# Performance work log

Hardware: AMD Instinct MI355X
Metric: run time of the kernel (lower is better)

The kernel has to match this reference:

```python
import jax, jax.numpy as jnp
import numpy as np

EPS = 1e-5

def _layer_norm(x, w, b):
    mu = jnp.mean(x, axis=-1, keepdims=True)
    var = jnp.mean((x - mu) ** 2, axis=-1, keepdims=True)
    return (x - mu) * jax.lax.rsqrt(var + EPS) * w + b

B, N, C, D = 8, 16384, 256, 2
K = 4096  # ceil(N / 4)

def setup_inputs() -> dict:
    key = jax.random.key(0)
    k0, k1, k2, k3 = jax.random.split(key, 4)
    pos = jax.random.uniform(k0, (B, N, D), dtype=jnp.float32)
    feat = jax.random.normal(k1, (B, N, C), dtype=jnp.float32)
    assignment = jax.random.randint(k2, (B, N), 0, K)
    norm_w = jnp.ones((C + D,), jnp.float32)
    norm_b = jnp.zeros((C + D,), jnp.float32)
    lin_w = jax.random.normal(k3, (2 * C, C + D), jnp.float32) * 0.02
    return {"pos": pos, "feat": feat, "assignment": assignment,
            "norm_w": norm_w, "norm_b": norm_b, "lin_w": lin_w}

def reference(pos, feat, assignment, norm_w, norm_b, lin_w):
    b, n, c = feat.shape
    d = pos.shape[2]
    k = K
    # normalize coordinates by per-dim global max
    pos = pos / jnp.max(pos.reshape(-1, d), axis=0)
    # flatten (batch, cluster) into segments for one big segment_sum
    seg = (assignment + jnp.arange(b, dtype=assignment.dtype)[:, None] * k).reshape(-1)  # [b*n]
    count = jax.ops.segment_sum(jnp.ones((b * n,), pos.dtype), seg,
                                num_segments=b * k).reshape(b, k)
    safe = jnp.maximum(count, 1.0)
    # cluster mean position (scatter_add + divide)
    mean_pos = jax.ops.segment_sum(pos.reshape(-1, d), seg,
                                   num_segments=b * k).reshape(b, k, d) / safe[..., None]
    # relative position via gather
    idx = jnp.broadcast_to(assignment[:, :, None], (b, n, d))
    rel_pos = pos - jnp.take_along_axis(mean_pos, idx, axis=1)
    # norm + linear (dim+pos_dim -> 2*dim, no bias)
    h = _layer_norm(jnp.concatenate([feat, rel_pos], axis=-1), norm_w, norm_b)
    h = jnp.einsum('bnf,of->bno', h, lin_w)  # [b, n, 2c]
    # cluster mean pooling of features (segment sum / count)
    merged = jax.ops.segment_sum(h.reshape(b * n, 2 * c), seg,
                                 num_segments=b * k).reshape(b, k, 2 * c) / safe[..., None]
    # zero out empty clusters and emit validity mask (valid_row_idx path)
    valid = (count > 0).astype(merged.dtype)  # [b, k]
    new_feat = merged * valid[..., None]
    new_pos = mean_pos * valid[..., None]
    new_mask = valid[..., None]  # [b, k, 1]
    return (new_pos, new_feat, new_mask)
```

## Files before the change

kernel.cpp:

```cpp
#include <hip/hip_runtime.h>

#define BB 8
#define NN 16384
#define CC 256
#define KK 4096
#define FDIM 258
#define FP 320
#define OC 512
#define NPTS (BB * NN)
#define NROWS (BB * KK)
#define CAP 64
#define LNEPS 1e-5f

#define OUT_FEAT_OFF 65536
#define OUT_MASK_OFF (65536 + 16777216)

#define OFF_MAX 0
#define OFF_ICOUNT 16
#define OFF_ACCH 32784
#define ACC_FSLOTS (NROWS * FP / 2)
#define OFF_INV (OFF_ACCH + ACC_FSLOTS)
#define OFF_LIST (OFF_INV + NROWS)
#define OFF_WPH (OFF_LIST + NROWS * CAP)
#define ZERO_FLOATS (OFF_ACCH + ACC_FSLOTS)

typedef _Float16 h8v __attribute__((ext_vector_type(8)));
typedef _Float16 h4v __attribute__((ext_vector_type(4)));
typedef float f4v __attribute__((ext_vector_type(4)));

__global__ void k_maxpos(const float* __restrict__ pos, float* ws) {
    int i = blockIdx.x * blockDim.x + threadIdx.x;
    float mx = 0.f, my = 0.f;
    for (; i < NPTS; i += gridDim.x * blockDim.x) {
        float2 p = ((const float2*)pos)[i];
        mx = fmaxf(mx, p.x);
        my = fmaxf(my, p.y);
    }
    for (int off = 32; off > 0; off >>= 1) {
        mx = fmaxf(mx, __shfl_down(mx, off));
        my = fmaxf(my, __shfl_down(my, off));
    }
    if ((threadIdx.x & 63) == 0) {
        atomicMax((int*)(ws + OFF_MAX + 0), __float_as_int(mx));
        atomicMax((int*)(ws + OFF_MAX + 1), __float_as_int(my));
    }
}

__global__ void k_count(const int* __restrict__ asg, float* ws) {
    int* icount = (int*)(ws + OFF_ICOUNT);
    int* list = (int*)(ws + OFF_LIST);
    int i = blockIdx.x * blockDim.x + threadIdx.x;
    for (; i < NPTS; i += gridDim.x * blockDim.x) {
        int b = i >> 14;
        int row = b * KK + asg[i];
        int slot = atomicAdd(icount + row, 1);
        if (slot < CAP) list[row * CAP + slot] = i;
    }
}

__global__ void k_padw(const float* __restrict__ lw, float* ws) {
    _Float16* Wh = (_Float16*)(ws + OFF_WPH);
    int i = blockIdx.x * blockDim.x + threadIdx.x;
    if (i >= OC * FP) return;
    int o = i / FP, f = i - o * FP;
    Wh[i] = (f < FDIM) ? (_Float16)lw[o * FDIM + f] : (_Float16)0.f;
}

__global__ __launch_bounds__(256) void k_gather(
    const float* __restrict__ feat, const float* __restrict__ pos,
    const float* __restrict__ nw, const float* __restrict__ nb,
    float* ws, float* __restrict__ out) {
    int t = threadIdx.x;
    int lane = t & 63;
    int row = (blockIdx.x << 2) + (t >> 6);
    const int* icount = (const int*)(ws + OFF_ICOUNT);
    const int* list = (const int*)(ws + OFF_LIST);
    _Float16* Ah = (_Float16*)(ws + OFF_ACCH);

    int cnt = icount[row];
    if (cnt > CAP) cnt = CAP;
    float fcnt = (float)cnt;
    float invc = 1.f / fmaxf(fcnt, 1.f);
    float mxx = ws[OFF_MAX + 0], mxy = ws[OFF_MAX + 1];

    int ptl = (lane < cnt) ? list[row * CAP + lane] : 0;
    float px = 0.f, py = 0.f;
    if (lane < cnt) {
        float2 p = ((const float2*)pos)[ptl];
        px = p.x / mxx;
        py = p.y / mxy;
    }
    float sx = px, sy = py;
    for (int m = 32; m; m >>= 1) {
        sx += __shfl_xor(sx, m);
        sy += __shfl_xor(sy, m);
    }
    float meanx = sx * invc, meany = sy * invc;
    float valid = (cnt > 0) ? 1.f : 0.f;
    if (lane == 0) {
        out[2 * row + 0] = meanx * valid;
        out[2 * row + 1] = meany * valid;
        out[OUT_MASK_OFF + row] = valid;
        ws[OFF_INV + row] = invc;
    }

    float a0 = 0.f, a1 = 0.f, a2 = 0.f, a3 = 0.f, arx = 0.f, ary = 0.f;
    for (int s = 0; s < cnt; ++s) {
        int pt = __shfl(ptl, s);
        float rx = __shfl(px, s) - meanx;
        float ry = __shfl(py, s) - meany;
        float4 v = ((const float4*)(feat + (size_t)pt * CC))[lane];
        float S = v.x + v.y + v.z + v.w;
        float Q = v.x * v.x + v.y * v.y + v.z * v.z + v.w * v.w;
        for (int m = 32; m; m >>= 1) {
            S += __shfl_xor(S, m);
            Q += __shfl_xor(Q, m);
        }
        S += rx + ry;
        Q += rx * rx + ry * ry;
        float mu = S * (1.f / FDIM);
        float var = Q * (1.f / FDIM) - mu * mu;
        float rs = rsqrtf(var + LNEPS);
        a0 += (v.x - mu) * rs;
        a1 += (v.y - mu) * rs;
        a2 += (v.z - mu) * rs;
        a3 += (v.w - mu) * rs;
        arx += (rx - mu) * rs;
        ary += (ry - mu) * rs;
    }
    float4 w4 = ((const float4*)nw)[lane];
    float4 b4 = ((const float4*)nb)[lane];
    h4v h;
    h[0] = (_Float16)(a0 * w4.x + fcnt * b4.x);
    h[1] = (_Float16)(a1 * w4.y + fcnt * b4.y);
    h[2] = (_Float16)(a2 * w4.z + fcnt * b4.z);
    h[3] = (_Float16)(a3 * w4.w + fcnt * b4.w);
    *(h4v*)(Ah + (size_t)row * FP + lane * 4) = h;
    if (lane == 0) {
        Ah[(size_t)row * FP + 256] = (_Float16)(arx * nw[256] + fcnt * nb[256]);
        Ah[(size_t)row * FP + 257] = (_Float16)(ary * nw[257] + fcnt * nb[257]);
    }
}

#define GM 128
#define GN 128
#define GK 64
#define LDK 72

__global__ __launch_bounds__(256) void k_gemm(const float* __restrict__ ws,
                                              float* __restrict__ out) {
    __shared__ _Float16 As[GM][LDK];
    __shared__ _Float16 Bs[GN][LDK];
    const _Float16* Ah = (const _Float16*)(ws + OFF_ACCH);
    const _Float16* Wh = (const _Float16*)(ws + OFF_WPH);
    const float* inv = ws + OFF_INV;

    int t = threadIdx.x;
    int lane = t & 63;
    int wv = t >> 6;
    int wr = wv & 1, wc = wv >> 1;
    int row0 = blockIdx.x * GM, col0 = blockIdx.y * GN;
    int l15 = lane & 15, kq = lane >> 4;

    f4v acc[4][4] = {};

    for (int k0 = 0; k0 < FP; k0 += GK) {
#pragma unroll
        for (int l = 0; l < 4; ++l) {
            int c = l * 256 + t;
            int r = c >> 3, kb = (c & 7) * 8;
            *(uint4*)&As[r][kb] = *(const uint4*)(Ah + (size_t)(row0 + r) * FP + k0 + kb);
            *(uint4*)&Bs[r][kb] = *(const uint4*)(Wh + (size_t)(col0 + r) * FP + k0 + kb);
        }
        __syncthreads();
#pragma unroll
        for (int ks = 0; ks < 2; ++ks) {
            h8v af[4], bf[4];
#pragma unroll
            for (int i = 0; i < 4; ++i)
                af[i] = *(const h8v*)&As[wr * 64 + i * 16 + l15][ks * 32 + kq * 8];
#pragma unroll
            for (int j = 0; j < 4; ++j)
                bf[j] = *(const h8v*)&Bs[wc * 64 + j * 16 + l15][ks * 32 + kq * 8];
#pragma unroll
            for (int i = 0; i < 4; ++i)
#pragma unroll
                for (int j = 0; j < 4; ++j)
                    acc[i][j] = __builtin_amdgcn_mfma_f32_16x16x32_f16(
                        af[i], bf[j], acc[i][j], 0, 0, 0);
        }
        __syncthreads();
    }

#pragma unroll
    for (int i = 0; i < 4; ++i) {
#pragma unroll
        for (int r = 0; r < 4; ++r) {
            int row = row0 + wr * 64 + i * 16 + kq * 4 + r;
            float sc = inv[row];
#pragma unroll
            for (int j = 0; j < 4; ++j) {
                int col = col0 + wc * 64 + j * 16 + l15;
                out[OUT_FEAT_OFF + (size_t)row * OC + col] = acc[i][j][r] * sc;
            }
        }
    }
}

extern "C" void kernel_launch(void* const* d_in, const int* in_sizes, int n_in,
                              void* d_out, int out_size, void* d_ws, size_t ws_size,
                              hipStream_t stream) {
    const float* pos = (const float*)d_in[0];
    const float* feat = (const float*)d_in[1];
    const int* asg = (const int*)d_in[2];
    const float* nw = (const float*)d_in[3];
    const float* nb = (const float*)d_in[4];
    const float* lw = (const float*)d_in[5];
    float* out = (float*)d_out;
    float* ws = (float*)d_ws;

    hipMemsetAsync(d_ws, 0, (size_t)ZERO_FLOATS * sizeof(float), stream);
    k_maxpos<<<512, 256, 0, stream>>>(pos, ws);
    k_count<<<1024, 256, 0, stream>>>(asg, ws);
    k_padw<<<(OC * FP + 255) / 256, 256, 0, stream>>>(lw, ws);
    k_gather<<<NROWS / 4, 256, 0, stream>>>(feat, pos, nw, nb, ws, out);
    k_gemm<<<dim3(NROWS / GM, OC / GN), 256, 0, stream>>>(ws, out);
}
```

Measured before the change: 317.0 us.

## Fuse prep kernels, shrink workspace memset, swizzle GEMM LDS tiles

Merges max-position, counting, and weight-padding into one prep kernel, removing two launches. The memset now clears only the max and count region; k_gather writes the zero padding columns of the activation buffer itself instead of relying on the large memset. The GEMM drops the padded LDS stride and uses an XOR swizzle on 16-byte chunks to avoid bank conflicts. The risk is in correctness of the padding writes and the swizzle indexing.

```diff
diff --git a/kernel.cpp b/kernel.cpp
--- a/kernel.cpp
+++ b/kernel.cpp
@@ -17,53 +17,53 @@
 
 #define OFF_MAX 0
 #define OFF_ICOUNT 16
+#define MEMSET_FLOATS (16 + NROWS)
 #define OFF_ACCH 32784
 #define ACC_FSLOTS (NROWS * FP / 2)
 #define OFF_INV (OFF_ACCH + ACC_FSLOTS)
 #define OFF_LIST (OFF_INV + NROWS)
 #define OFF_WPH (OFF_LIST + NROWS * CAP)
-#define ZERO_FLOATS (OFF_ACCH + ACC_FSLOTS)
 
 typedef _Float16 h8v __attribute__((ext_vector_type(8)));
 typedef _Float16 h4v __attribute__((ext_vector_type(4)));
 typedef float f4v __attribute__((ext_vector_type(4)));
 
-__global__ void k_maxpos(const float* __restrict__ pos, float* ws) {
-    int i = blockIdx.x * blockDim.x + threadIdx.x;
-    float mx = 0.f, my = 0.f;
-    for (; i < NPTS; i += gridDim.x * blockDim.x) {
+#define PREP_PB 512
+#define PREP_WB 160
+
+__global__ __launch_bounds__(256) void k_prep(const float* __restrict__ pos,
+                                              const int* __restrict__ asg,
+                                              const float* __restrict__ lw,
+                                              float* ws) {
+    int bid = blockIdx.x;
+    if (bid < PREP_PB) {
+        int i = bid * 256 + threadIdx.x;
+        int* icount = (int*)(ws + OFF_ICOUNT);
+        int* list = (int*)(ws + OFF_LIST);
         float2 p = ((const float2*)pos)[i];
-        mx = fmaxf(mx, p.x);
-        my = fmaxf(my, p.y);
-    }
-    for (int off = 32; off > 0; off >>= 1) {
-        mx = fmaxf(mx, __shfl_down(mx, off));
-        my = fmaxf(my, __shfl_down(my, off));
-    }
-    if ((threadIdx.x & 63) == 0) {
-        atomicMax((int*)(ws + OFF_MAX + 0), __float_as_int(mx));
-        atomicMax((int*)(ws + OFF_MAX + 1), __float_as_int(my));
-    }
-}
-
-__global__ void k_count(const int* __restrict__ asg, float* ws) {
-    int* icount = (int*)(ws + OFF_ICOUNT);
-    int* list = (int*)(ws + OFF_LIST);
-    int i = blockIdx.x * blockDim.x + threadIdx.x;
-    for (; i < NPTS; i += gridDim.x * blockDim.x) {
         int b = i >> 14;
         int row = b * KK + asg[i];
         int slot = atomicAdd(icount + row, 1);
         if (slot < CAP) list[row * CAP + slot] = i;
-    }
-}
-
-__global__ void k_padw(const float* __restrict__ lw, float* ws) {
-    _Float16* Wh = (_Float16*)(ws + OFF_WPH);
-    int i = blockIdx.x * blockDim.x + threadIdx.x;
-    if (i >= OC * FP) return;
-    int o = i / FP, f = i - o * FP;
-    Wh[i] = (f < FDIM) ? (_Float16)lw[o * FDIM + f] : (_Float16)0.f;
+        float mx = p.x, my = p.y;
+        for (int off = 32; off > 0; off >>= 1) {
+            mx = fmaxf(mx, __shfl_down(mx, off));
+            my = fmaxf(my, __shfl_down(my, off));
+        }
+        if ((threadIdx.x & 63) == 0) {
+            atomicMax((int*)(ws + OFF_MAX + 0), __float_as_int(mx));
+            atomicMax((int*)(ws + OFF_MAX + 1), __float_as_int(my));
+        }
+    } else {
+        _Float16* Wh = (_Float16*)(ws + OFF_WPH);
+        int e = ((bid - PREP_PB) * 256 + threadIdx.x) * 4;
+        int o = e / FP, f = e - o * FP;
+        h4v h;
+#pragma unroll
+        for (int u = 0; u < 4; ++u)
+            h[u] = (f + u < FDIM) ? (_Float16)lw[o * FDIM + f + u] : (_Float16)0.f;
+        *(h4v*)(Wh + e) = h;
+    }
 }
 
 __global__ __launch_bounds__(256) void k_gather(
@@ -136,21 +136,24 @@
     h[2] = (_Float16)(a2 * w4.z + fcnt * b4.z);
     h[3] = (_Float16)(a3 * w4.w + fcnt * b4.w);
     *(h4v*)(Ah + (size_t)row * FP + lane * 4) = h;
-    if (lane == 0) {
-        Ah[(size_t)row * FP + 256] = (_Float16)(arx * nw[256] + fcnt * nb[256]);
-        Ah[(size_t)row * FP + 257] = (_Float16)(ary * nw[257] + fcnt * nb[257]);
+    if (lane >= 16 && lane < 32) {
+        h4v z = {};
+        if (lane == 16) {
+            z[0] = (_Float16)(arx * nw[256] + fcnt * nb[256]);
+            z[1] = (_Float16)(ary * nw[257] + fcnt * nb[257]);
+        }
+        *(h4v*)(Ah + (size_t)row * FP + 256 + (lane - 16) * 4) = z;
     }
 }
 
 #define GM 128
 #define GN 128
 #define GK 64
-#define LDK 72
 
 __global__ __launch_bounds__(256) void k_gemm(const float* __restrict__ ws,
                                               float* __restrict__ out) {
-    __shared__ _Float16 As[GM][LDK];
-    __shared__ _Float16 Bs[GN][LDK];
+    __shared__ _Float16 As[GM][GK];
+    __shared__ _Float16 Bs[GN][GK];
     const _Float16* Ah = (const _Float16*)(ws + OFF_ACCH);
     const _Float16* Wh = (const _Float16*)(ws + OFF_WPH);
     const float* inv = ws + OFF_INV;
@@ -161,6 +164,7 @@
     int wr = wv & 1, wc = wv >> 1;
     int row0 = blockIdx.x * GM, col0 = blockIdx.y * GN;
     int l15 = lane & 15, kq = lane >> 4;
+    int sw = l15 & 7;
 
     f4v acc[4][4] = {};
 
@@ -168,20 +172,22 @@
 #pragma unroll
         for (int l = 0; l < 4; ++l) {
             int c = l * 256 + t;
-            int r = c >> 3, kb = (c & 7) * 8;
-            *(uint4*)&As[r][kb] = *(const uint4*)(Ah + (size_t)(row0 + r) * FP + k0 + kb);
-            *(uint4*)&Bs[r][kb] = *(const uint4*)(Wh + (size_t)(col0 + r) * FP + k0 + kb);
+            int r = c >> 3, ch = c & 7;
+            int pc = ch ^ (r & 7);
+            *(uint4*)&As[r][pc * 8] = *(const uint4*)(Ah + (size_t)(row0 + r) * FP + k0 + ch * 8);
+            *(uint4*)&Bs[r][pc * 8] = *(const uint4*)(Wh + (size_t)(col0 + r) * FP + k0 + ch * 8);
         }
         __syncthreads();
 #pragma unroll
         for (int ks = 0; ks < 2; ++ks) {
             h8v af[4], bf[4];
+            int lc = ((ks << 2) | kq);
 #pragma unroll
             for (int i = 0; i < 4; ++i)
-                af[i] = *(const h8v*)&As[wr * 64 + i * 16 + l15][ks * 32 + kq * 8];
+                af[i] = *(const h8v*)&As[wr * 64 + i * 16 + l15][(lc ^ sw) * 8];
 #pragma unroll
             for (int j = 0; j < 4; ++j)
-                bf[j] = *(const h8v*)&Bs[wc * 64 + j * 16 + l15][ks * 32 + kq * 8];
+                bf[j] = *(const h8v*)&Bs[wc * 64 + j * 16 + l15][(lc ^ sw) * 8];
 #pragma unroll
             for (int i = 0; i < 4; ++i)
 #pragma unroll
@@ -219,10 +225,8 @@
     float* out = (float*)d_out;
     float* ws = (float*)d_ws;
 
-    hipMemsetAsync(d_ws, 0, (size_t)ZERO_FLOATS * sizeof(float), stream);
-    k_maxpos<<<512, 256, 0, stream>>>(pos, ws);
-    k_count<<<1024, 256, 0, stream>>>(asg, ws);
-    k_padw<<<(OC * FP + 255) / 256, 256, 0, stream>>>(lw, ws);
+    hipMemsetAsync(d_ws, 0, (size_t)MEMSET_FLOATS * sizeof(float), stream);
+    k_prep<<<PREP_PB + PREP_WB, 256, 0, stream>>>(pos, asg, lw, ws);
     k_gather<<<NROWS / 4, 256, 0, stream>>>(feat, pos, nw, nb, ws, out);
     k_gemm<<<dim3(NROWS / GM, OC / GN), 256, 0, stream>>>(ws, out);
 }
```

After: 311.0 us. No clear change (-1.9%).
